# Kernel optimization log

Hardware: AMD Instinct MI355X
Metric: run time of the kernel (lower is better)

## Reference

```python
import jax, jax.numpy as jnp
import numpy as np

HID, H, HKV, D, INT, S, T = 2048, 16, 8, 128, 6144, 4096, 512
POS = 0          # absolute position of the first token in this prefill chunk
EPS = 1e-6
SCALE = 1.0 / D ** 0.5
REP = H // HKV


def setup_inputs() -> dict:
    key = jax.random.key(0)
    ks = jax.random.split(key, 12)
    w = lambda k, sh: jax.random.normal(k, sh, dtype=jnp.float32) * 0.02

    hidden_conv = jax.random.normal(ks[0], (1, HID, 1, T), dtype=jnp.float32)

    # RoPE tables for absolute positions POS..POS+T-1, HF half-rotation layout
    inv_freq = 1.0 / (10000.0 ** (jnp.arange(0, D, 2, dtype=jnp.float32) / D))
    pos = (POS + jnp.arange(T, dtype=jnp.float32))
    ang = pos[:, None] * inv_freq[None, :]                      # (T, D/2)
    emb = jnp.concatenate([ang, ang], axis=-1)                  # (T, D)
    cos = jnp.cos(emb)[None]                                    # (1, T, D)
    sin = jnp.sin(emb)[None]

    # one-hot write mask: column t has a 1 at row POS+t
    update_mask = jnp.zeros((S, T), jnp.float32).at[POS + jnp.arange(T), jnp.arange(T)].set(1.0)[None, None]
    # causal mask over the cache: slot s visible to token t iff s <= POS+t
    attn_mask = jnp.where(jnp.arange(S)[None, :] <= (POS + jnp.arange(T))[:, None], 0.0, -1e4).astype(jnp.float32)[None, None]

    k_cache = jnp.zeros((1, HKV, S, D), jnp.float32)
    v_cache = jnp.zeros((1, HKV, S, D), jnp.float32)

    return dict(
        hidden_conv=hidden_conv, cos=cos, sin=sin,
        update_mask=update_mask, attn_mask=attn_mask,
        k_cache=k_cache, v_cache=v_cache,
        wq=w(ks[1], (H * D, HID)), wk=w(ks[2], (HKV * D, HID)),
        wv=w(ks[3], (HKV * D, HID)), wo=w(ks[4], (HID, H * D)),
        ln1_w=jnp.ones((HID,), jnp.float32), ln2_w=jnp.ones((HID,), jnp.float32),
        qn_w=jnp.ones((D,), jnp.float32), kn_w=jnp.ones((D,), jnp.float32),
        w_gate_up=w(ks[5], (2 * INT, HID)), w_down=w(ks[6], (HID, INT)),
    )


def _rms(x, w):
    return x * jax.lax.rsqrt(jnp.mean(x * x, axis=-1, keepdims=True) + EPS) * w


def _rotate_half(x):
    x1, x2 = jnp.split(x, 2, axis=-1)
    return jnp.concatenate([-x2, x1], axis=-1)


def reference(hidden_conv, cos, sin, update_mask, attn_mask, k_cache, v_cache,
              wq, wk, wv, wo, ln1_w, ln2_w, qn_w, kn_w, w_gate_up, w_down):
    # (1, HID, 1, T) conv layout -> (1, T, HID)
    x = jnp.transpose(hidden_conv[:, :, 0, :], (0, 2, 1))

    h = _rms(x, ln1_w)
    # 1x1 conv == linear; channel order h*D+d matches view(1,H,D,T)
    q = jnp.einsum('btc,oc->bto', h, wq).reshape(1, T, H, D).transpose(0, 2, 1, 3)    # (1,H,T,D)
    k = jnp.einsum('btc,oc->bto', h, wk).reshape(1, T, HKV, D).transpose(0, 2, 1, 3)  # (1,HKV,T,D)
    v = jnp.einsum('btc,oc->bto', h, wv).reshape(1, T, HKV, D).transpose(0, 2, 1, 3)

    q = _rms(q, qn_w)
    k = _rms(k, kn_w)

    cos_b = cos[:, None]  # (1,1,T,D)
    sin_b = sin[:, None]
    q = q * cos_b + _rotate_half(q) * sin_b
    k = k * cos_b + _rotate_half(k) * sin_b

    # matmul-based KV cache write via one-hot mask (faithful to original)
    k_inc = jnp.matmul(update_mask, k)                 # (1,HKV,S,D)
    v_inc = jnp.matmul(update_mask, v)
    write_any = jnp.sum(update_mask, axis=-1, keepdims=True)  # (1,1,S,1)
    k_full = k_cache * (1.0 - write_any) + k_inc
    v_full = v_cache * (1.0 - write_any) + v_inc

    k_rep = jnp.repeat(k_full, REP, axis=1)            # (1,H,S,D)
    v_rep = jnp.repeat(v_full, REP, axis=1)

    scores = jnp.einsum('bhtd,bhsd->bhts', q, k_rep) * SCALE + attn_mask  # (1,H,T,S)
    attn = jax.nn.softmax(scores, axis=-1)
    out = jnp.einsum('bhts,bhsd->bhtd', attn, v_rep)   # (1,H,T,D)

    o_in = out.transpose(0, 2, 1, 3).reshape(1, T, H * D)
    attn_out = jnp.einsum('btc,oc->bto', o_in, wo)
    hidden = x + attn_out

    h2 = _rms(hidden, ln2_w)
    gate_up = jnp.einsum('btc,oc->bto', h2, w_gate_up)
    gate, up = jnp.split(gate_up, 2, axis=-1)
    mlp = jnp.einsum('bti,oi->bto', jax.nn.silu(gate) * up, w_down)
    hidden = hidden + mlp

    hidden_out = jnp.transpose(hidden, (0, 2, 1))[:, :, None, :]  # back to (1,HID,1,T)
    return hidden_out, k_full, v_full


if __name__ == '__main__':
    outs = reference(**setup_inputs())
    print([o.shape for o in outs])
```

## Files before the change

### kernel.cpp

```cpp
#include <hip/hip_runtime.h>
#include <hip/hip_bf16.h>
#include <hip/hip_fp16.h>

#define TT 512
#define HIDD 2048
#define NH 16
#define NKV 8
#define DD 128
#define INTR 6144
#define SEQ 4096
#define SCALE 0.08838834764831845f

typedef __attribute__((ext_vector_type(8))) short short8;
typedef __attribute__((ext_vector_type(4))) float floatx4;

static __device__ __forceinline__ unsigned short f2b(float f) {
  unsigned int u = __float_as_uint(f);
  u += 0x7fffu + ((u >> 16) & 1u);
  return (unsigned short)(u >> 16);
}

static __device__ __forceinline__ unsigned int f2b2(float a, float b) {
  __hip_bfloat162 h = __float22bfloat162_rn(make_float2(a, b));
  return *reinterpret_cast<unsigned int*>(&h);
}


template <int BM, bool H> struct TR;
template <> struct TR<128, true>  { short8 v[2]; };
template <> struct TR<128, false> { float4 v[4]; };
template <> struct TR<64, true>   { short8 v[1]; };
template <> struct TR<64, false>  { float4 v[2]; };

template <int BM, bool H>
static __device__ __forceinline__ void tile_load(const void* __restrict__ src, int ld, int k0,
                                                 int tid, TR<BM, H>& r) {
  if constexpr (H) {
    const unsigned short* s = (const unsigned short*)src;
    const int r0 = tid >> 2, c8 = (tid & 3) << 3;
#pragma unroll
    for (int i = 0; i < BM / 64; ++i)
      r.v[i] = *reinterpret_cast<const short8*>(s + (size_t)(r0 + (i << 6)) * ld + k0 + c8);
  } else {
    const float* s = (const float*)src;
    const int r0 = tid >> 2, c8 = (tid & 3) << 3;
#pragma unroll
    for (int i = 0; i < BM / 64; ++i) {
      const float* p = s + (size_t)(r0 + (i << 6)) * ld + k0 + c8;
      r.v[2 * i]     = *reinterpret_cast<const float4*>(p);
      r.v[2 * i + 1] = *reinterpret_cast<const float4*>(p + 4);
    }
  }
}

template <int BM, bool H>
static __device__ __forceinline__ void tile_store(const TR<BM, H>& r, unsigned short* dst, int tid) {
  if constexpr (H) {
    const int r0 = tid >> 2, c8 = (tid & 3) << 3;
#pragma unroll
    for (int i = 0; i < BM / 64; ++i)
      *reinterpret_cast<short8*>(dst + (r0 + (i << 6)) * 40 + c8) = r.v[i];
  } else {
    const int r0 = tid >> 2, c8 = (tid & 3) << 3;
#pragma unroll
    for (int i = 0; i < BM / 64; ++i) {
      uint4 o;
      o.x = f2b2(r.v[2 * i].x,     r.v[2 * i].y);
      o.y = f2b2(r.v[2 * i].z,     r.v[2 * i].w);
      o.z = f2b2(r.v[2 * i + 1].x, r.v[2 * i + 1].y);
      o.w = f2b2(r.v[2 * i + 1].z, r.v[2 * i + 1].w);
      *reinterpret_cast<uint4*>(dst + (r0 + (i << 6)) * 40 + c8) = o;
    }
  }
}

template <int BM, bool A16, bool B16>
static __device__ __forceinline__ void gemm_core(const void* __restrict__ A, int lda,
                                                 const void* __restrict__ B, int ldb,
                                                 int kbeg, int kend, floatx4 (&acc)[BM / 32][4],
                                                 unsigned short* As, unsigned short* Bs) {
  constexpr int MI = BM / 32;
  const int tid = threadIdx.x;
  const int lane = tid & 63;
  const int wave = tid >> 6;
  const int wr = (wave >> 1) * (BM >> 1);
  const int wc = (wave & 1) << 6;
  const int lrow = lane & 15;
  const int koff = (lane >> 4) << 3;
  TR<BM, A16> ra;
  TR<128, B16> rb;
  tile_load<BM, A16>(A, lda, kbeg, tid, ra);
  tile_load<128, B16>(B, ldb, kbeg, tid, rb);
  tile_store<BM, A16>(ra, As, tid);
  tile_store<128, B16>(rb, Bs, tid);
  if (kbeg + 32 < kend) {
    tile_load<BM, A16>(A, lda, kbeg + 32, tid, ra);
    tile_load<128, B16>(B, ldb, kbeg + 32, tid, rb);
  }
  __syncthreads();
  int p = 0;
  for (int k0 = kbeg; k0 < kend; k0 += 32) {
    const unsigned short* Ac = As + p * (BM * 40);
    const unsigned short* Bc = Bs + p * (128 * 40);
    unsigned short* An = As + (p ^ 1) * (BM * 40);
    unsigned short* Bn = Bs + (p ^ 1) * (128 * 40);
    short8 af[MI], bfr[4];
#pragma unroll
    for (int mi = 0; mi < MI; ++mi)
      af[mi] = *reinterpret_cast<const short8*>(Ac + (wr + mi * 16 + lrow) * 40 + koff);
#pragma unroll
    for (int ni = 0; ni < 4; ++ni)
      bfr[ni] = *reinterpret_cast<const short8*>(Bc + (wc + ni * 16 + lrow) * 40 + koff);
    if (k0 + 32 < kend) {
      tile_store<BM, A16>(ra, An, tid);
      tile_store<128, B16>(rb, Bn, tid);
      if (k0 + 64 < kend) {
        tile_load<BM, A16>(A, lda, k0 + 64, tid, ra);
        tile_load<128, B16>(B, ldb, k0 + 64, tid, rb);
      }
    }
#pragma unroll
    for (int mi = 0; mi < MI; ++mi)
#pragma unroll
      for (int ni = 0; ni < 4; ++ni)
        acc[mi][ni] = __builtin_amdgcn_mfma_f32_16x16x32_bf16(af[mi], bfr[ni], acc[mi][ni], 0, 0, 0);
    __syncthreads();
    p ^= 1;
  }
}

#define EPI_VARS \
  const int lane = threadIdx.x & 63; \
  const int wave = threadIdx.x >> 6; \
  const int wc = (wave & 1) << 6;    \
  const int lrow = lane & 15;        \
  const int quad = lane >> 4;

#define ZERO_ACC(MI_) \
  floatx4 acc[MI_][4]; \
  _Pragma("unroll") for (int mi = 0; mi < MI_; ++mi) \
  _Pragma("unroll") for (int ni = 0; ni < 4; ++ni) { floatx4 z = {0.f, 0.f, 0.f, 0.f}; acc[mi][ni] = z; }

template <int S>
static __device__ __forceinline__ void swz(int b, int& mt, int& nt, int& s) {
  mt = (b >> 3) & 3;
  const int gid = ((b >> 5) << 3) | (b & 7);
  nt = gid / S;
  s = gid - nt * S;
}


__global__ __launch_bounds__(1024) void k_rms1(const float* __restrict__ conv,
                                               const float* __restrict__ w,
                                               float* __restrict__ xb,
                                               unsigned short* __restrict__ h1b) {
  const int t0 = blockIdx.x << 5;
  const int tid = threadIdx.x;
  const int j = tid & 31;
  const int g = tid >> 5;
  __shared__ float part[32][32];
  __shared__ float tile[32][33];
  __shared__ float rs[32];
  float ss = 0.f;
  for (int c0 = 0; c0 < HIDD; c0 += 32) {
    const float v = conv[(size_t)(c0 + g) * TT + t0 + j];
    ss += v * v;
  }
  part[g][j] = ss;
  __syncthreads();
  if (g == 0) {
    float tot = 0.f;
#pragma unroll
    for (int q = 0; q < 32; ++q) tot += part[q][j];
    rs[j] = rsqrtf(tot * (1.0f / HIDD) + 1e-6f);
  }
  __syncthreads();
  for (int c0 = 0; c0 < HIDD; c0 += 32) {
    tile[g][j] = conv[(size_t)(c0 + g) * TT + t0 + j];
    __syncthreads();
    const float v = tile[j][g];
    const float rv = rs[g];
    xb[(size_t)(t0 + g) * HIDD + c0 + j] = v;
    h1b[(size_t)(t0 + g) * HIDD + c0 + j] = f2b(v * rv * w[c0 + j]);
    __syncthreads();
  }
}

__global__ __launch_bounds__(256) void k_gemm_qkv(const unsigned short* __restrict__ h1b,
                                                  const float* __restrict__ wq,
                                                  const float* __restrict__ wk,
                                                  const float* __restrict__ wv,
                                                  float* __restrict__ Pq) {
  __shared__ unsigned short As[2 * 128 * 40], Bs[2 * 128 * 40];
  int mt, nt, s;
  swz<4>(blockIdx.x, mt, nt, s);
  const int m0 = mt << 7, n0 = nt << 7;
  const float* Bp;
  if (n0 < 2048)      Bp = wq + (size_t)n0 * HIDD;
  else if (n0 < 3072) Bp = wk + (size_t)(n0 - 2048) * HIDD;
  else                Bp = wv + (size_t)(n0 - 3072) * HIDD;
  ZERO_ACC(4)
  gemm_core<128, true, false>(h1b + (size_t)m0 * HIDD, HIDD, Bp, HIDD, s * 512, s * 512 + 512, acc, As, Bs);
  EPI_VARS
  const int wr = (wave >> 1) << 6;
  float* out = Pq + (size_t)s * (TT * 4096);
#pragma unroll
  for (int mi = 0; mi < 4; ++mi)
#pragma unroll
    for (int ni = 0; ni < 4; ++ni)
#pragma unroll
      for (int rr = 0; rr < 4; ++rr) {
        const int row = m0 + wr + mi * 16 + quad * 4 + rr;
        const int col = n0 + wc + ni * 16 + lrow;
        out[(size_t)row * 4096 + col] = acc[mi][ni][rr];
      }
}

__global__ __launch_bounds__(128) void k_rope(const float* __restrict__ Pq,
                                              const float* __restrict__ cosb,
                                              const float* __restrict__ sinb,
                                              const float* __restrict__ qnw,
                                              const float* __restrict__ knw,
                                              unsigned short* __restrict__ qb,
                                              unsigned short* __restrict__ kb,
                                              unsigned short* __restrict__ vtb,
                                              float* __restrict__ kout,
                                              float* __restrict__ vout) {
  const int u = blockIdx.x;
  const int t = blockIdx.y;
  const int d = threadIdx.x;
  __shared__ float red[2];
  __shared__ float sh[DD];
  int slot;
  if (u < NH)            slot = u * DD + d;
  else if (u < NH + NKV) slot = 2048 + (u - NH) * DD + d;
  else                   slot = 3072 + (u - NH - NKV) * DD + d;
  const size_t idx = (size_t)t * 4096 + slot;
  float val = Pq[idx] + Pq[idx + TT * 4096] + Pq[idx + 2 * TT * 4096] + Pq[idx + 3 * TT * 4096];
  if (u < NH + NKV) {
    float ss = val * val;
    const int lane = d & 63, wid = d >> 6;
#pragma unroll
    for (int o = 32; o; o >>= 1) ss += __shfl_xor(ss, o);
    if (!lane) red[wid] = ss;
    __syncthreads();
    const float r = rsqrtf((red[0] + red[1]) * (1.0f / DD) + 1e-6f);
    const float w = (u < NH) ? qnw[d] : knw[d];
    const float nv = val * r * w;
    sh[d] = nv;
    __syncthreads();
    const float partner = sh[d ^ 64];
    const float rh = (d < 64) ? -partner : partner;
    const float o = nv * cosb[(size_t)t * DD + d] + rh * sinb[(size_t)t * DD + d];
    if (u < NH) {
      qb[(size_t)u * TT * DD + (size_t)t * DD + d] = f2b(o);
    } else {
      const int kh = u - NH;
      kout[(size_t)kh * SEQ * DD + (size_t)t * DD + d] = o;
      kb[(size_t)kh * TT * DD + (size_t)t * DD + d] = f2b(o);
    }
  } else {
    const int vh = u - NH - NKV;
    vout[(size_t)vh * SEQ * DD + (size_t)t * DD + d] = val;
    vtb[(size_t)vh * DD * TT + (size_t)d * TT + t] = f2b(val);
  }
}

__global__ __launch_bounds__(256) void k_tail(const float* __restrict__ kc,
                                              const float* __restrict__ vc,
                                              float* __restrict__ ko,
                                              float* __restrict__ vo) {
  const int i = blockIdx.x * 256 + threadIdx.x;
  const int e = i << 2;
  const int s = (e >> 7) & (SEQ - 1);
  if (s >= TT) {
    reinterpret_cast<float4*>(ko)[i] = reinterpret_cast<const float4*>(kc)[i];
    reinterpret_cast<float4*>(vo)[i] = reinterpret_cast<const float4*>(vc)[i];
  }
}

__global__ __launch_bounds__(256) void k_scores(const unsigned short* __restrict__ qb,
                                                const unsigned short* __restrict__ kb,
                                                float* __restrict__ sc) {
  __shared__ unsigned short As[2 * 64 * 40], Bs[2 * 128 * 40];
  const int m0 = blockIdx.x << 6, n0 = blockIdx.y << 7, h = blockIdx.z;
  ZERO_ACC(2)
  gemm_core<64, true, true>(qb + (size_t)h * TT * DD + (size_t)m0 * DD, DD,
                            kb + (size_t)(h >> 1) * TT * DD + (size_t)n0 * DD, DD, 0, DD, acc, As, Bs);
  EPI_VARS
  const int wr = (wave >> 1) << 5;
  float* out = sc + (size_t)h * TT * TT;
#pragma unroll
  for (int mi = 0; mi < 2; ++mi)
#pragma unroll
    for (int ni = 0; ni < 4; ++ni)
#pragma unroll
      for (int rr = 0; rr < 4; ++rr) {
        const int t = m0 + wr + mi * 16 + quad * 4 + rr;
        const int s = n0 + wc + ni * 16 + lrow;
        float v = acc[mi][ni][rr] * SCALE;
        if (s > t) v += -10000.0f;
        out[(size_t)t * TT + s] = v;
      }
}

__global__ __launch_bounds__(256) void k_softmax(const float* __restrict__ sc,
                                                 unsigned short* __restrict__ Pb) {
  const int h = blockIdx.x >> 9, t = blockIdx.x & 511;
  const int tid = threadIdx.x;
  const float* row = sc + ((size_t)h * TT + t) * TT;
  float v0 = row[tid], v1 = row[tid + 256];
  __shared__ float red[4];
  const int lane = tid & 63, wid = tid >> 6;
  float m = fmaxf(v0, v1);
#pragma unroll
  for (int o = 32; o; o >>= 1) m = fmaxf(m, __shfl_xor(m, o));
  if (!lane) red[wid] = m;
  __syncthreads();
  m = fmaxf(fmaxf(red[0], red[1]), fmaxf(red[2], red[3]));
  const float e0 = __expf(v0 - m), e1 = __expf(v1 - m);
  float s = e0 + e1;
  __syncthreads();
#pragma unroll
  for (int o = 32; o; o >>= 1) s += __shfl_xor(s, o);
  if (!lane) red[wid] = s;
  __syncthreads();
  const float inv = 1.0f / (red[0] + red[1] + red[2] + red[3]);
  unsigned short* orow = Pb + ((size_t)h * TT + t) * TT;
  orow[tid] = f2b(e0 * inv);
  orow[tid + 256] = f2b(e1 * inv);
}

__global__ __launch_bounds__(256) void k_pv(const unsigned short* __restrict__ Pb,
                                            const unsigned short* __restrict__ vtb,
                                            float* __restrict__ Ppv) {
  __shared__ unsigned short As[2 * 64 * 40], Bs[2 * 128 * 40];
  const int m0 = blockIdx.x << 6, h = blockIdx.y, s = blockIdx.z;
  ZERO_ACC(2)
  gemm_core<64, true, true>(Pb + (size_t)h * TT * TT + (size_t)m0 * TT, TT,
                            vtb + (size_t)(h >> 1) * DD * TT, TT, s * 128, s * 128 + 128, acc, As, Bs);
  EPI_VARS
  const int wr = (wave >> 1) << 5;
  float* out = Ppv + (size_t)s * (TT * HIDD);
#pragma unroll
  for (int mi = 0; mi < 2; ++mi)
#pragma unroll
    for (int ni = 0; ni < 4; ++ni)
#pragma unroll
      for (int rr = 0; rr < 4; ++rr) {
        const int row = m0 + wr + mi * 16 + quad * 4 + rr;
        const int col = wc + ni * 16 + lrow;
        out[(size_t)row * HIDD + h * DD + col] = acc[mi][ni][rr];
      }
}

__global__ __launch_bounds__(256) void k_red_pv(const float* __restrict__ Ppv,
                                                unsigned short* __restrict__ o_inb) {
  const int i = blockIdx.x * 256 + threadIdx.x;
  const float4* p = reinterpret_cast<const float4*>(Ppv);
  float4 a = p[i];
  const float4 b = p[i + 262144], c = p[i + 524288], d = p[i + 786432];
  a.x += b.x + c.x + d.x; a.y += b.y + c.y + d.y;
  a.z += b.z + c.z + d.z; a.w += b.w + c.w + d.w;
  uint2 o;
  o.x = f2b2(a.x, a.y);
  o.y = f2b2(a.z, a.w);
  *reinterpret_cast<uint2*>(o_inb + (size_t)i * 4) = o;
}

__global__ __launch_bounds__(256) void k_gemm_o(const unsigned short* __restrict__ o_inb,
                                                const float* __restrict__ wo,
                                                float* __restrict__ Po) {
  __shared__ unsigned short As[2 * 128 * 40], Bs[2 * 128 * 40];
  int mt, nt, s;
  swz<8>(blockIdx.x, mt, nt, s);
  const int m0 = mt << 7, n0 = nt << 7;
  ZERO_ACC(4)
  gemm_core<128, true, false>(o_inb + (size_t)m0 * HIDD, HIDD, wo + (size_t)n0 * HIDD, HIDD,
                              s * 256, s * 256 + 256, acc, As, Bs);
  EPI_VARS
  const int wr = (wave >> 1) << 6;
  float* out = Po + (size_t)s * (TT * HIDD);
#pragma unroll
  for (int mi = 0; mi < 4; ++mi)
#pragma unroll
    for (int ni = 0; ni < 4; ++ni)
#pragma unroll
      for (int rr = 0; rr < 4; ++rr) {
        const int row = m0 + wr + mi * 16 + quad * 4 + rr;
        const int col = n0 + wc + ni * 16 + lrow;
        out[(size_t)row * HIDD + col] = acc[mi][ni][rr];
      }
}

__global__ __launch_bounds__(256) void k_rms2(const float* __restrict__ xb,
                                              const float* __restrict__ Po,
                                              const float* __restrict__ w,
                                              float* __restrict__ hidden,
                                              unsigned short* __restrict__ h2b) {
  const int t = blockIdx.x;
  const int tid = threadIdx.x;
  float2 v[4];
  float ss = 0.f;
#pragma unroll
  for (int i = 0; i < 4; ++i) {
    const int c = (tid << 1) + (i << 9);
    const size_t idx = (size_t)t * HIDD + c;
    float2 a = *reinterpret_cast<const float2*>(xb + idx);
#pragma unroll
    for (int sp = 0; sp < 8; ++sp) {
      const float2 b = *reinterpret_cast<const float2*>(Po + idx + (size_t)sp * (TT * HIDD));
      a.x += b.x; a.y += b.y;
    }
    v[i] = a;
    ss += a.x * a.x + a.y * a.y;
  }
  __shared__ float red[4];
  const int lane = tid & 63, wid = tid >> 6;
#pragma unroll
  for (int o = 32; o; o >>= 1) ss += __shfl_xor(ss, o);
  if (!lane) red[wid] = ss;
  __syncthreads();
  const float tot = red[0] + red[1] + red[2] + red[3];
  const float r = rsqrtf(tot * (1.0f / HIDD) + 1e-6f);
#pragma unroll
  for (int i = 0; i < 4; ++i) {
    const int c = (tid << 1) + (i << 9);
    const size_t idx = (size_t)t * HIDD + c;
    *reinterpret_cast<float2*>(hidden + idx) = v[i];
    const float2 wv2 = *reinterpret_cast<const float2*>(w + c);
    *reinterpret_cast<unsigned int*>(h2b + idx) = f2b2(v[i].x * r * wv2.x, v[i].y * r * wv2.y);
  }
}

__global__ __launch_bounds__(256) void k_gemm_gu(const unsigned short* __restrict__ h2b,
                                                 const float* __restrict__ wgu,
                                                 __half* __restrict__ guh) {
  __shared__ unsigned short As[2 * 128 * 40], Bs[2 * 128 * 40];
  int mt, nt, s;
  swz<2>(blockIdx.x, mt, nt, s);
  const int m0 = mt << 7, n0 = nt << 7;
  ZERO_ACC(4)
  gemm_core<128, true, false>(h2b + (size_t)m0 * HIDD, HIDD, wgu + (size_t)n0 * HIDD, HIDD,
                              s * 1024, s * 1024 + 1024, acc, As, Bs);
  EPI_VARS
  const int wr = (wave >> 1) << 6;
  __half* out = guh + (size_t)s * (TT * 2 * INTR);
#pragma unroll
  for (int mi = 0; mi < 4; ++mi)
#pragma unroll
    for (int ni = 0; ni < 4; ++ni)
#pragma unroll
      for (int rr = 0; rr < 4; ++rr) {
        const int row = m0 + wr + mi * 16 + quad * 4 + rr;
        const int col = n0 + wc + ni * 16 + lrow;
        out[(size_t)row * (2 * INTR) + col] = __float2half(acc[mi][ni][rr]);
      }
}

__global__ __launch_bounds__(256) void k_silu(const __half* __restrict__ guh,
                                              unsigned short* __restrict__ actb) {
  const int j0 = (blockIdx.x * 256 + threadIdx.x) << 1;
  const int t = blockIdx.y;
  const size_t base = (size_t)t * (2 * INTR) + j0;
  const size_t off = (size_t)TT * (2 * INTR);
  const float2 g0 = __half22float2(*reinterpret_cast<const __half2*>(guh + base));
  const float2 g1 = __half22float2(*reinterpret_cast<const __half2*>(guh + off + base));
  const float2 u0 = __half22float2(*reinterpret_cast<const __half2*>(guh + base + INTR));
  const float2 u1 = __half22float2(*reinterpret_cast<const __half2*>(guh + off + base + INTR));
  const float gx = g0.x + g1.x, gy = g0.y + g1.y;
  const float ux = u0.x + u1.x, uy = u0.y + u1.y;
  const float a0 = gx / (1.f + __expf(-gx)) * ux;
  const float a1 = gy / (1.f + __expf(-gy)) * uy;
  *reinterpret_cast<unsigned int*>(actb + (size_t)t * INTR + j0) = f2b2(a0, a1);
}

__global__ __launch_bounds__(256) void k_gemm_down(const unsigned short* __restrict__ actb,
                                                   const float* __restrict__ wdn,
                                                   float* __restrict__ Pdn) {
  __shared__ unsigned short As[2 * 128 * 40], Bs[2 * 128 * 40];
  int mt, nt, s;
  swz<8>(blockIdx.x, mt, nt, s);
  const int m0 = mt << 7, n0 = nt << 7;
  ZERO_ACC(4)
  gemm_core<128, true, false>(actb + (size_t)m0 * INTR, INTR, wdn + (size_t)n0 * INTR, INTR,
                              s * 768, s * 768 + 768, acc, As, Bs);
  EPI_VARS
  const int wr = (wave >> 1) << 6;
  float* out = Pdn + (size_t)s * (TT * HIDD);
#pragma unroll
  for (int mi = 0; mi < 4; ++mi)
#pragma unroll
    for (int ni = 0; ni < 4; ++ni)
#pragma unroll
      for (int rr = 0; rr < 4; ++rr) {
        const int row = m0 + wr + mi * 16 + quad * 4 + rr;
        const int col = n0 + wc + ni * 16 + lrow;
        out[(size_t)row * HIDD + col] = acc[mi][ni][rr];
      }
}

__global__ __launch_bounds__(256) void k_final(const float* __restrict__ hidden,
                                               const float* __restrict__ Pdn,
                                               float* __restrict__ out0) {
  __shared__ float tile[32][33];
  const int c0 = blockIdx.x << 5, t0 = blockIdx.y << 5;
  const int tx = threadIdx.x & 31, ty0 = (threadIdx.x >> 5) << 2;
#pragma unroll
  for (int i = 0; i < 4; ++i) {
    const int t = t0 + ty0 + i;
    const size_t idx = (size_t)t * HIDD + c0 + tx;
    float a = hidden[idx];
#pragma unroll
    for (int sp = 0; sp < 8; ++sp) a += Pdn[idx + (size_t)sp * (TT * HIDD)];
    tile[ty0 + i][tx] = a;
  }
  __syncthreads();
#pragma unroll
  for (int i = 0; i < 4; ++i)
    out0[(size_t)(c0 + ty0 + i) * TT + t0 + tx] = tile[tx][ty0 + i];
}

extern "C" void kernel_launch(void* const* d_in, const int* in_sizes, int n_in,
                              void* d_out, int out_size, void* d_ws, size_t ws_size,
                              hipStream_t stream) {
  const float* conv   = (const float*)d_in[0];
  const float* cosb   = (const float*)d_in[1];
  const float* sinb   = (const float*)d_in[2];
  const float* kcache = (const float*)d_in[5];
  const float* vcache = (const float*)d_in[6];
  const float* wq  = (const float*)d_in[7];
  const float* wk  = (const float*)d_in[8];
  const float* wv  = (const float*)d_in[9];
  const float* wo  = (const float*)d_in[10];
  const float* ln1 = (const float*)d_in[11];
  const float* ln2 = (const float*)d_in[12];
  const float* qnw = (const float*)d_in[13];
  const float* knw = (const float*)d_in[14];
  const float* wgu = (const float*)d_in[15];
  const float* wdn = (const float*)d_in[16];

  float* ws = (float*)d_ws;
  float* xb = ws + 0;
  unsigned short* h1b  = (unsigned short*)(ws + 1048576);
  unsigned short* o_inb = h1b;
  unsigned short* h2b  = (unsigned short*)(ws + 1572864);
  float* hidden = ws + 2097152;
  unsigned short* qb  = (unsigned short*)(ws + 3145728);
  unsigned short* kb  = qb + 1048576;
  unsigned short* vtb = kb + 524288;
  unsigned short* actb = (unsigned short*)(ws + 4194304);
  float* R   = ws + 5767168;
  float* Pq  = R;
  unsigned short* Pb = (unsigned short*)R;
  float* sc  = R + 2097152;
  float* Ppv = R + 2097152;
  float* Po  = R;
  __half* guh = (__half*)R;
  float* Pdn = R;

  float* out0 = (float*)d_out;
  float* kout = out0 + 1048576;
  float* vout = kout + 4194304;

  k_rms1<<<16, 1024, 0, stream>>>(conv, ln1, xb, h1b);
  k_gemm_qkv<<<512, 256, 0, stream>>>(h1b, wq, wk, wv, Pq);
  k_rope<<<dim3(NH + 2 * NKV, TT), 128, 0, stream>>>(Pq, cosb, sinb, qnw, knw, qb, kb, vtb, kout, vout);
  k_tail<<<4096, 256, 0, stream>>>(kcache, vcache, kout, vout);
  k_scores<<<dim3(8, 4, NH), 256, 0, stream>>>(qb, kb, sc);
  k_softmax<<<NH * TT, 256, 0, stream>>>(sc, Pb);
  k_pv<<<dim3(8, NH, 4), 256, 0, stream>>>(Pb, vtb, Ppv);
  k_red_pv<<<1024, 256, 0, stream>>>(Ppv, o_inb);
  k_gemm_o<<<512, 256, 0, stream>>>(o_inb, wo, Po);
  k_rms2<<<TT, 256, 0, stream>>>(xb, Po, ln2, hidden, h2b);
  k_gemm_gu<<<768, 256, 0, stream>>>(h2b, wgu, guh);
  k_silu<<<dim3(12, TT), 256, 0, stream>>>(guh, actb);
  k_gemm_down<<<512, 256, 0, stream>>>(actb, wdn, Pdn);
  k_final<<<dim3(HIDD / 32, TT / 32), 256, 0, stream>>>(hidden, Pdn, out0);
}
```

Baseline: 479.6 us.

## Deepen GEMM pipeline with two register stages and a manually unrolled ping-pong

Restructures the GEMM main loop to hold two sets of prefetch registers and unroll by two k-steps. Global loads for step k+64 are issued before the MFMA work, and the LDS store of the already-loaded tile is placed after it. The goal is to hide global memory latency more fully and drop the index arithmetic for swapping LDS buffers. The cost is higher register pressure, which may lower occupancy. Barriers become a raw s_barrier after lgkmcnt(0) rather than __syncthreads. The unrolled loop assumes the K range is a multiple of 64.

```diff
diff --git a/kernel.cpp b/kernel.cpp
--- a/kernel.cpp
+++ b/kernel.cpp
@@ -73,6 +73,33 @@
     }
   }
 }
+
+#define GSTEP(PA_, PB_, CURA_, CURB_, NXTA_, NXTB_, SA_, SB_, KC_)                         \
+  {                                                                                        \
+    const int knx_ = (KC_) + 64;                                                           \
+    if (knx_ < kend) {                                                                     \
+      tile_load<BM, A16>(A, lda, knx_, tid, NXTA_);                                        \
+      tile_load<128, B16>(B, ldb, knx_, tid, NXTB_);                                       \
+    }                                                                                      \
+    short8 af[MI], bfr[4];                                                                 \
+    _Pragma("unroll")                                                                      \
+    for (int mi = 0; mi < MI; ++mi)                                                        \
+      af[mi] = *reinterpret_cast<const short8*>((PA_) + (wr + mi * 16 + lrow) * 40 + koff);\
+    _Pragma("unroll")                                                                      \
+    for (int ni = 0; ni < 4; ++ni)                                                         \
+      bfr[ni] = *reinterpret_cast<const short8*>((PB_) + (wc + ni * 16 + lrow) * 40 + koff);\
+    _Pragma("unroll")                                                                      \
+    for (int mi = 0; mi < MI; ++mi)                                                        \
+      _Pragma("unroll")                                                                    \
+      for (int ni = 0; ni < 4; ++ni)                                                       \
+        acc[mi][ni] = __builtin_amdgcn_mfma_f32_16x16x32_bf16(af[mi], bfr[ni], acc[mi][ni], 0, 0, 0); \
+    if ((KC_) + 32 < kend) {                                                               \
+      tile_store<BM, A16>(CURA_, SA_, tid);                                                \
+      tile_store<128, B16>(CURB_, SB_, tid);                                               \
+    }                                                                                      \
+    asm volatile("s_waitcnt lgkmcnt(0)" ::: "memory");                                     \
+    __builtin_amdgcn_s_barrier();                                                          \
+  }
 
 template <int BM, bool A16, bool B16>
 static __device__ __forceinline__ void gemm_core(const void* __restrict__ A, int lda,
@@ -87,47 +114,25 @@
   const int wc = (wave & 1) << 6;
   const int lrow = lane & 15;
   const int koff = (lane >> 4) << 3;
-  TR<BM, A16> ra;
-  TR<128, B16> rb;
-  tile_load<BM, A16>(A, lda, kbeg, tid, ra);
-  tile_load<128, B16>(B, ldb, kbeg, tid, rb);
-  tile_store<BM, A16>(ra, As, tid);
-  tile_store<128, B16>(rb, Bs, tid);
-  if (kbeg + 32 < kend) {
-    tile_load<BM, A16>(A, lda, kbeg + 32, tid, ra);
-    tile_load<128, B16>(B, ldb, kbeg + 32, tid, rb);
-  }
-  __syncthreads();
-  int p = 0;
-  for (int k0 = kbeg; k0 < kend; k0 += 32) {
-    const unsigned short* Ac = As + p * (BM * 40);
-    const unsigned short* Bc = Bs + p * (128 * 40);
-    unsigned short* An = As + (p ^ 1) * (BM * 40);
-    unsigned short* Bn = Bs + (p ^ 1) * (128 * 40);
-    short8 af[MI], bfr[4];
-#pragma unroll
-    for (int mi = 0; mi < MI; ++mi)
-      af[mi] = *reinterpret_cast<const short8*>(Ac + (wr + mi * 16 + lrow) * 40 + koff);
-#pragma unroll
-    for (int ni = 0; ni < 4; ++ni)
-      bfr[ni] = *reinterpret_cast<const short8*>(Bc + (wc + ni * 16 + lrow) * 40 + koff);
-    if (k0 + 32 < kend) {
-      tile_store<BM, A16>(ra, An, tid);
-      tile_store<128, B16>(rb, Bn, tid);
-      if (k0 + 64 < kend) {
-        tile_load<BM, A16>(A, lda, k0 + 64, tid, ra);
-        tile_load<128, B16>(B, ldb, k0 + 64, tid, rb);
-      }
-    }
-#pragma unroll
-    for (int mi = 0; mi < MI; ++mi)
-#pragma unroll
-      for (int ni = 0; ni < 4; ++ni)
-        acc[mi][ni] = __builtin_amdgcn_mfma_f32_16x16x32_bf16(af[mi], bfr[ni], acc[mi][ni], 0, 0, 0);
-    __syncthreads();
-    p ^= 1;
-  }
-}
+  unsigned short* As1 = As + BM * 40;
+  unsigned short* Bs1 = Bs + 128 * 40;
+  TR<BM, A16> ra0, ra1;
+  TR<128, B16> rb0, rb1;
+  tile_load<BM, A16>(A, lda, kbeg, tid, ra0);
+  tile_load<128, B16>(B, ldb, kbeg, tid, rb0);
+  tile_load<BM, A16>(A, lda, kbeg + 32, tid, ra1);
+  tile_load<128, B16>(B, ldb, kbeg + 32, tid, rb1);
+  tile_store<BM, A16>(ra0, As, tid);
+  tile_store<128, B16>(rb0, Bs, tid);
+  asm volatile("s_waitcnt lgkmcnt(0)" ::: "memory");
+  __builtin_amdgcn_s_barrier();
+  for (int k0 = kbeg; k0 < kend; k0 += 64) {
+    GSTEP(As,  Bs,  ra1, rb1, ra0, rb0, As1, Bs1, k0)
+    GSTEP(As1, Bs1, ra0, rb0, ra1, rb1, As,  Bs,  k0 + 32)
+  }
+}
+
+#undef GSTEP
 
 #define EPI_VARS \
   const int lane = threadIdx.x & 63; \
```

Result: slower. 495.5 us (+3.3%).

## Stage GEMM tiles with direct global-to-LDS loads and keep fp32 weights in LDS

Applied to the files above, without the earlier changes.

The shared GEMM core now copies tiles straight from global memory into LDS with global_load_lds, replacing the register load, convert and store path. Waits use explicit vmcnt counts and raw barriers in a double-buffered pipeline. fp32 weight tiles sit in LDS with an XOR swizzle and are converted to bf16 when fragments are read, so the B-side LDS footprint doubles. Every GEMM kernel (QKV, scores, PV, O, gate-up, down) moves to this path, which aims to cut register pressure and staging instructions at the cost of more LDS traffic and per-fragment conversion work.

```diff
diff --git a/kernel.cpp b/kernel.cpp
--- a/kernel.cpp
+++ b/kernel.cpp
@@ -26,106 +26,128 @@
 }
 
 
-template <int BM, bool H> struct TR;
-template <> struct TR<128, true>  { short8 v[2]; };
-template <> struct TR<128, false> { float4 v[4]; };
-template <> struct TR<64, true>   { short8 v[1]; };
-template <> struct TR<64, false>  { float4 v[2]; };
-
-template <int BM, bool H>
-static __device__ __forceinline__ void tile_load(const void* __restrict__ src, int ld, int k0,
-                                                 int tid, TR<BM, H>& r) {
-  if constexpr (H) {
-    const unsigned short* s = (const unsigned short*)src;
-    const int r0 = tid >> 2, c8 = (tid & 3) << 3;
-#pragma unroll
-    for (int i = 0; i < BM / 64; ++i)
-      r.v[i] = *reinterpret_cast<const short8*>(s + (size_t)(r0 + (i << 6)) * ld + k0 + c8);
+static __device__ __forceinline__ void gld16(const void* g, void* l) {
+  __builtin_amdgcn_global_load_lds(
+      (const __attribute__((address_space(1))) unsigned int*)g,
+      (__attribute__((address_space(3))) unsigned int*)l, 16, 0, 0);
+}
+
+template <int BM, bool B16>
+static __device__ __forceinline__ void stage_tile(const unsigned short* __restrict__ A, int lda,
+                                                  const void* __restrict__ B, int ldb, int k0,
+                                                  unsigned char* buf, int wave, int lane) {
+  {
+    const int rpw = BM >> 2;
+    const int rl = lane >> 2;
+    const int c8 = (lane & 3) << 3;
+#pragma unroll
+    for (int i = 0; i < BM / 64; ++i) {
+      const int rbase = wave * rpw + i * 16;
+      gld16(A + (size_t)(rbase + rl) * lda + k0 + c8, buf + (size_t)rbase * 64);
+    }
+  }
+  unsigned char* Bb = buf + BM * 64;
+  if constexpr (B16) {
+    const unsigned short* Bh = (const unsigned short*)B;
+    const int rl = lane >> 2;
+    const int c8 = (lane & 3) << 3;
+#pragma unroll
+    for (int i = 0; i < 2; ++i) {
+      const int rbase = wave * 32 + i * 16;
+      gld16(Bh + (size_t)(rbase + rl) * ldb + k0 + c8, Bb + (size_t)rbase * 64);
+    }
   } else {
-    const float* s = (const float*)src;
-    const int r0 = tid >> 2, c8 = (tid & 3) << 3;
-#pragma unroll
-    for (int i = 0; i < BM / 64; ++i) {
-      const float* p = s + (size_t)(r0 + (i << 6)) * ld + k0 + c8;
-      r.v[2 * i]     = *reinterpret_cast<const float4*>(p);
-      r.v[2 * i + 1] = *reinterpret_cast<const float4*>(p + 4);
+    const float* Bf = (const float*)B;
+    const int rl = lane >> 3;
+    const int sp = lane & 7;
+#pragma unroll
+    for (int i = 0; i < 4; ++i) {
+      const int rbase = wave * 32 + i * 8;
+      const int r = rbase + rl;
+      gld16(Bf + (size_t)r * ldb + k0 + ((sp ^ (r & 7)) << 2), Bb + (size_t)rbase * 128);
     }
   }
 }
 
-template <int BM, bool H>
-static __device__ __forceinline__ void tile_store(const TR<BM, H>& r, unsigned short* dst, int tid) {
-  if constexpr (H) {
-    const int r0 = tid >> 2, c8 = (tid & 3) << 3;
-#pragma unroll
-    for (int i = 0; i < BM / 64; ++i)
-      *reinterpret_cast<short8*>(dst + (r0 + (i << 6)) * 40 + c8) = r.v[i];
+template <int BM, bool B16>
+static __device__ __forceinline__ void frags_from(const unsigned char* buf, int wr, int wc,
+                                                  int lrow, int koff,
+                                                  short8 (&af)[BM / 32], short8 (&bfr)[4]) {
+  const unsigned short* Ab = (const unsigned short*)buf;
+#pragma unroll
+  for (int mi = 0; mi < BM / 32; ++mi)
+    af[mi] = *reinterpret_cast<const short8*>(Ab + (size_t)(wr + mi * 16 + lrow) * 32 + koff);
+  if constexpr (B16) {
+    const unsigned short* Bb = (const unsigned short*)(buf + BM * 64);
+#pragma unroll
+    for (int ni = 0; ni < 4; ++ni)
+      bfr[ni] = *reinterpret_cast<const short8*>(Bb + (size_t)(wc + ni * 16 + lrow) * 32 + koff);
   } else {
-    const int r0 = tid >> 2, c8 = (tid & 3) << 3;
-#pragma unroll
-    for (int i = 0; i < BM / 64; ++i) {
-      uint4 o;
-      o.x = f2b2(r.v[2 * i].x,     r.v[2 * i].y);
-      o.y = f2b2(r.v[2 * i].z,     r.v[2 * i].w);
-      o.z = f2b2(r.v[2 * i + 1].x, r.v[2 * i + 1].y);
-      o.w = f2b2(r.v[2 * i + 1].z, r.v[2 * i + 1].w);
-      *reinterpret_cast<uint4*>(dst + (r0 + (i << 6)) * 40 + c8) = o;
+    const float* Bf = (const float*)(buf + BM * 64);
+    const int s0 = koff >> 2;
+#pragma unroll
+    for (int ni = 0; ni < 4; ++ni) {
+      const int r = wc + ni * 16 + lrow;
+      const float4 x = *reinterpret_cast<const float4*>(Bf + (size_t)r * 32 + ((s0 ^ (r & 7)) << 2));
+      const float4 y = *reinterpret_cast<const float4*>(Bf + (size_t)r * 32 + (((s0 + 1) ^ (r & 7)) << 2));
+      union { short8 s; unsigned int u[4]; } pk;
+      pk.u[0] = f2b2(x.x, x.y); pk.u[1] = f2b2(x.z, x.w);
+      pk.u[2] = f2b2(y.x, y.y); pk.u[3] = f2b2(y.z, y.w);
+      bfr[ni] = pk.s;
     }
   }
 }
 
-template <int BM, bool A16, bool B16>
-static __device__ __forceinline__ void gemm_core(const void* __restrict__ A, int lda,
+template <int BM, bool B16>
+static __device__ __forceinline__ void gemm_core(const unsigned short* __restrict__ A, int lda,
                                                  const void* __restrict__ B, int ldb,
                                                  int kbeg, int kend, floatx4 (&acc)[BM / 32][4],
-                                                 unsigned short* As, unsigned short* Bs) {
+                                                 unsigned char* Ls) {
   constexpr int MI = BM / 32;
+  constexpr int TILE = BM * 64 + (B16 ? 8192 : 16384);
+  constexpr int NB = (BM / 64) + (B16 ? 2 : 4);
   const int tid = threadIdx.x;
-  const int lane = tid & 63;
-  const int wave = tid >> 6;
+  const int lane = tid & 63, wave = tid >> 6;
   const int wr = (wave >> 1) * (BM >> 1);
   const int wc = (wave & 1) << 6;
   const int lrow = lane & 15;
   const int koff = (lane >> 4) << 3;
-  TR<BM, A16> ra;
-  TR<128, B16> rb;
-  tile_load<BM, A16>(A, lda, kbeg, tid, ra);
-  tile_load<128, B16>(B, ldb, kbeg, tid, rb);
-  tile_store<BM, A16>(ra, As, tid);
-  tile_store<128, B16>(rb, Bs, tid);
-  if (kbeg + 32 < kend) {
-    tile_load<BM, A16>(A, lda, kbeg + 32, tid, ra);
-    tile_load<128, B16>(B, ldb, kbeg + 32, tid, rb);
-  }
-  __syncthreads();
+  const int NT = (kend - kbeg) >> 5;
+  stage_tile<BM, B16>(A, lda, B, ldb, kbeg,      Ls,        wave, lane);
+  stage_tile<BM, B16>(A, lda, B, ldb, kbeg + 32, Ls + TILE, wave, lane);
   int p = 0;
-  for (int k0 = kbeg; k0 < kend; k0 += 32) {
-    const unsigned short* Ac = As + p * (BM * 40);
-    const unsigned short* Bc = Bs + p * (128 * 40);
-    unsigned short* An = As + (p ^ 1) * (BM * 40);
-    unsigned short* Bn = Bs + (p ^ 1) * (128 * 40);
+  for (int t = 0; t < NT - 1; ++t) {
+    if constexpr (NB == 6)      asm volatile("s_waitcnt vmcnt(6)" ::: "memory");
+    else if constexpr (NB == 3) asm volatile("s_waitcnt vmcnt(3)" ::: "memory");
+    else if constexpr (NB == 4) asm volatile("s_waitcnt vmcnt(4)" ::: "memory");
+    else                        asm volatile("s_waitcnt vmcnt(5)" ::: "memory");
+    __builtin_amdgcn_sched_barrier(0);
+    __builtin_amdgcn_s_barrier();
     short8 af[MI], bfr[4];
-#pragma unroll
-    for (int mi = 0; mi < MI; ++mi)
-      af[mi] = *reinterpret_cast<const short8*>(Ac + (wr + mi * 16 + lrow) * 40 + koff);
-#pragma unroll
-    for (int ni = 0; ni < 4; ++ni)
-      bfr[ni] = *reinterpret_cast<const short8*>(Bc + (wc + ni * 16 + lrow) * 40 + koff);
-    if (k0 + 32 < kend) {
-      tile_store<BM, A16>(ra, An, tid);
-      tile_store<128, B16>(rb, Bn, tid);
-      if (k0 + 64 < kend) {
-        tile_load<BM, A16>(A, lda, k0 + 64, tid, ra);
-        tile_load<128, B16>(B, ldb, k0 + 64, tid, rb);
-      }
-    }
+    frags_from<BM, B16>(Ls + p * TILE, wr, wc, lrow, koff, af, bfr);
+    asm volatile("s_waitcnt lgkmcnt(0)" ::: "memory");
+    __builtin_amdgcn_sched_barrier(0);
+    __builtin_amdgcn_s_barrier();
+    if (t + 2 < NT)
+      stage_tile<BM, B16>(A, lda, B, ldb, kbeg + (t + 2) * 32, Ls + p * TILE, wave, lane);
 #pragma unroll
     for (int mi = 0; mi < MI; ++mi)
 #pragma unroll
       for (int ni = 0; ni < 4; ++ni)
         acc[mi][ni] = __builtin_amdgcn_mfma_f32_16x16x32_bf16(af[mi], bfr[ni], acc[mi][ni], 0, 0, 0);
-    __syncthreads();
     p ^= 1;
+  }
+  asm volatile("s_waitcnt vmcnt(0)" ::: "memory");
+  __builtin_amdgcn_sched_barrier(0);
+  __builtin_amdgcn_s_barrier();
+  {
+    short8 af[MI], bfr[4];
+    frags_from<BM, B16>(Ls + p * TILE, wr, wc, lrow, koff, af, bfr);
+#pragma unroll
+    for (int mi = 0; mi < MI; ++mi)
+#pragma unroll
+      for (int ni = 0; ni < 4; ++ni)
+        acc[mi][ni] = __builtin_amdgcn_mfma_f32_16x16x32_bf16(af[mi], bfr[ni], acc[mi][ni], 0, 0, 0);
   }
 }
 
@@ -191,7 +213,7 @@
                                                   const float* __restrict__ wk,
                                                   const float* __restrict__ wv,
                                                   float* __restrict__ Pq) {
-  __shared__ unsigned short As[2 * 128 * 40], Bs[2 * 128 * 40];
+  __shared__ __align__(16) unsigned char Ls[2 * (128 * 64 + 16384)];
   int mt, nt, s;
   swz<4>(blockIdx.x, mt, nt, s);
   const int m0 = mt << 7, n0 = nt << 7;
@@ -200,7 +222,7 @@
   else if (n0 < 3072) Bp = wk + (size_t)(n0 - 2048) * HIDD;
   else                Bp = wv + (size_t)(n0 - 3072) * HIDD;
   ZERO_ACC(4)
-  gemm_core<128, true, false>(h1b + (size_t)m0 * HIDD, HIDD, Bp, HIDD, s * 512, s * 512 + 512, acc, As, Bs);
+  gemm_core<128, false>(h1b + (size_t)m0 * HIDD, HIDD, Bp, HIDD, s * 512, s * 512 + 512, acc, Ls);
   EPI_VARS
   const int wr = (wave >> 1) << 6;
   float* out = Pq + (size_t)s * (TT * 4096);
@@ -282,11 +304,11 @@
 __global__ __launch_bounds__(256) void k_scores(const unsigned short* __restrict__ qb,
                                                 const unsigned short* __restrict__ kb,
                                                 float* __restrict__ sc) {
-  __shared__ unsigned short As[2 * 64 * 40], Bs[2 * 128 * 40];
+  __shared__ __align__(16) unsigned char Ls[2 * (64 * 64 + 8192)];
   const int m0 = blockIdx.x << 6, n0 = blockIdx.y << 7, h = blockIdx.z;
   ZERO_ACC(2)
-  gemm_core<64, true, true>(qb + (size_t)h * TT * DD + (size_t)m0 * DD, DD,
-                            kb + (size_t)(h >> 1) * TT * DD + (size_t)n0 * DD, DD, 0, DD, acc, As, Bs);
+  gemm_core<64, true>(qb + (size_t)h * TT * DD + (size_t)m0 * DD, DD,
+                      kb + (size_t)(h >> 1) * TT * DD + (size_t)n0 * DD, DD, 0, DD, acc, Ls);
   EPI_VARS
   const int wr = (wave >> 1) << 5;
   float* out = sc + (size_t)h * TT * TT;
@@ -334,11 +356,11 @@
 __global__ __launch_bounds__(256) void k_pv(const unsigned short* __restrict__ Pb,
                                             const unsigned short* __restrict__ vtb,
                                             float* __restrict__ Ppv) {
-  __shared__ unsigned short As[2 * 64 * 40], Bs[2 * 128 * 40];
+  __shared__ __align__(16) unsigned char Ls[2 * (64 * 64 + 8192)];
   const int m0 = blockIdx.x << 6, h = blockIdx.y, s = blockIdx.z;
   ZERO_ACC(2)
-  gemm_core<64, true, true>(Pb + (size_t)h * TT * TT + (size_t)m0 * TT, TT,
-                            vtb + (size_t)(h >> 1) * DD * TT, TT, s * 128, s * 128 + 128, acc, As, Bs);
+  gemm_core<64, true>(Pb + (size_t)h * TT * TT + (size_t)m0 * TT, TT,
+                      vtb + (size_t)(h >> 1) * DD * TT, TT, s * 128, s * 128 + 128, acc, Ls);
   EPI_VARS
   const int wr = (wave >> 1) << 5;
   float* out = Ppv + (size_t)s * (TT * HIDD);
@@ -371,13 +393,13 @@
 __global__ __launch_bounds__(256) void k_gemm_o(const unsigned short* __restrict__ o_inb,
                                                 const float* __restrict__ wo,
                                                 float* __restrict__ Po) {
-  __shared__ unsigned short As[2 * 128 * 40], Bs[2 * 128 * 40];
+  __shared__ __align__(16) unsigned char Ls[2 * (128 * 64 + 16384)];
   int mt, nt, s;
   swz<8>(blockIdx.x, mt, nt, s);
   const int m0 = mt << 7, n0 = nt << 7;
   ZERO_ACC(4)
-  gemm_core<128, true, false>(o_inb + (size_t)m0 * HIDD, HIDD, wo + (size_t)n0 * HIDD, HIDD,
-                              s * 256, s * 256 + 256, acc, As, Bs);
+  gemm_core<128, false>(o_inb + (size_t)m0 * HIDD, HIDD, wo + (size_t)n0 * HIDD, HIDD,
+                        s * 256, s * 256 + 256, acc, Ls);
   EPI_VARS
   const int wr = (wave >> 1) << 6;
   float* out = Po + (size_t)s * (TT * HIDD);
@@ -436,13 +458,13 @@
 __global__ __launch_bounds__(256) void k_gemm_gu(const unsigned short* __restrict__ h2b,
                                                  const float* __restrict__ wgu,
                                                  __half* __restrict__ guh) {
-  __shared__ unsigned short As[2 * 128 * 40], Bs[2 * 128 * 40];
+  __shared__ __align__(16) unsigned char Ls[2 * (128 * 64 + 16384)];
   int mt, nt, s;
   swz<2>(blockIdx.x, mt, nt, s);
   const int m0 = mt << 7, n0 = nt << 7;
   ZERO_ACC(4)
-  gemm_core<128, true, false>(h2b + (size_t)m0 * HIDD, HIDD, wgu + (size_t)n0 * HIDD, HIDD,
-                              s * 1024, s * 1024 + 1024, acc, As, Bs);
+  gemm_core<128, false>(h2b + (size_t)m0 * HIDD, HIDD, wgu + (size_t)n0 * HIDD, HIDD,
+                        s * 1024, s * 1024 + 1024, acc, Ls);
   EPI_VARS
   const int wr = (wave >> 1) << 6;
   __half* out = guh + (size_t)s * (TT * 2 * INTR);
@@ -478,13 +500,13 @@
 __global__ __launch_bounds__(256) void k_gemm_down(const unsigned short* __restrict__ actb,
                                                    const float* __restrict__ wdn,
                                                    float* __restrict__ Pdn) {
-  __shared__ unsigned short As[2 * 128 * 40], Bs[2 * 128 * 40];
+  __shared__ __align__(16) unsigned char Ls[2 * (128 * 64 + 16384)];
   int mt, nt, s;
   swz<8>(blockIdx.x, mt, nt, s);
   const int m0 = mt << 7, n0 = nt << 7;
   ZERO_ACC(4)
-  gemm_core<128, true, false>(actb + (size_t)m0 * INTR, INTR, wdn + (size_t)n0 * INTR, INTR,
-                              s * 768, s * 768 + 768, acc, As, Bs);
+  gemm_core<128, false>(actb + (size_t)m0 * INTR, INTR, wdn + (size_t)n0 * INTR, INTR,
+                        s * 768, s * 768 + 768, acc, Ls);
   EPI_VARS
   const int wr = (wave >> 1) << 6;
   float* out = Pdn + (size_t)s * (TT * HIDD);
```

After: 465.4 us. -3.0%, faster.
